# Kernel optimization log

Measured on AMD Instinct MI355X. Metric: run time of the kernel, lower is better.

The kernel has to match this reference:

```python
import jax, jax.numpy as jnp
import numpy as np

B, N, D, H, R = 4, 2048, 256, 8, 64
DH = D // H          # head dim = 32
K_SPARSE = 32        # top-k neighbors kept per query row
BN_EPS = 1e-5


def setup_inputs() -> dict:
    key = jax.random.key(0)
    ks = jax.random.split(key, 16)
    s_in = 1.0 / np.sqrt(D)
    s_r = 1.0 / np.sqrt(R)
    def lr(k1, k2):
        return (jax.random.normal(k1, (D, R), jnp.float32) * s_in,
                jax.random.normal(k2, (R, D), jnp.float32) * s_r)
    U_np, V_np = lr(ks[0], ks[1])
    U_q, V_q = lr(ks[2], ks[3])
    U_k, V_k = lr(ks[4], ks[5])
    U_v, V_v = lr(ks[6], ks[7])
    U_o, V_o = lr(ks[8], ks[9])
    U_op, V_op = lr(ks[10], ks[11])
    return {
        'x': jax.random.normal(ks[12], (B, N, D), jnp.float32),
        'U_np': U_np, 'V_np': V_np, 'b_np': jnp.zeros((D,), jnp.float32),
        'U_q': U_q, 'V_q': V_q,
        'U_k': U_k, 'V_k': V_k,
        'U_v': U_v, 'V_v': V_v,
        'U_o': U_o, 'V_o': V_o, 'b_o': jnp.zeros((D,), jnp.float32),
        'U_op': U_op, 'V_op': V_op, 'b_op': jnp.zeros((D,), jnp.float32),
        'gamma': jnp.ones((D,), jnp.float32),
        'beta': jnp.zeros((D,), jnp.float32),
    }


def _low_rank(x, U, V, b=None):
    y = (x @ U) @ V  # [..., D] -> [..., R] -> [..., D]
    return y + b if b is not None else y


def _heads(t):  # [B,N,D] -> [B,H,N,DH]
    return t.reshape(B, N, H, DH).transpose(0, 2, 1, 3)


def reference(x, U_np, V_np, b_np, U_q, V_q, U_k, V_k, U_v, V_v,
              U_o, V_o, b_o, U_op, V_op, b_op, gamma, beta):
    # node_proj: low-rank projection
    h = _low_rank(x, U_np, V_np, b_np)                      # [B,N,D]
    # low-rank sparse attention (q=k=v=h)
    q = _heads(_low_rank(h, U_q, V_q))                      # [B,H,N,DH]
    k = _heads(_low_rank(h, U_k, V_k))
    v = _heads(_low_rank(h, U_v, V_v))
    scores = jnp.einsum('bhnd,bhmd->bhnm', q, k) / jnp.sqrt(jnp.float32(DH))
    # topk sparsity: keep the K_SPARSE largest scores per query row
    thr = jax.lax.top_k(scores, K_SPARSE)[0][..., -1:]      # [B,H,N,1]
    neg_inf = jnp.finfo(scores.dtype).min
    scores = jnp.where(scores >= thr, scores, neg_inf)
    attn = jax.nn.softmax(scores, axis=-1)                  # [B,H,N,N]
    o = jnp.einsum('bhnm,bhmd->bhnd', attn, v)              # [B,H,N,DH]
    o = o.transpose(0, 2, 1, 3).reshape(B, N, D)
    o = _low_rank(o, U_o, V_o, b_o)                         # attention out proj
    # out_proj
    out = _low_rank(o, U_op, V_op, b_op)                    # [B,N,D]
    # BatchNorm1d over channel dim (stats over B and N, training-mode batch stats)
    mu = out.mean(axis=(0, 1))
    var = out.var(axis=(0, 1))
    out = (out - mu) * jax.lax.rsqrt(var + BN_EPS) * gamma + beta
    return out
```

## Files before the change

kernel.cpp:

```cpp
#include <hip/hip_runtime.h>
#include <hip/hip_bf16.h>

#define BB 4
#define NN 2048
#define DD 256
#define HH 8
#define RR 64
#define DHH 32
#define KSP 32
#define ROWS (BB*NN)
#define NEG_INF (-3.0e38f)

typedef __attribute__((ext_vector_type(8))) short bf16x8;
typedef __attribute__((ext_vector_type(4))) float f32x4;
#define MFMA16(A,B,C) __builtin_amdgcn_mfma_f32_16x16x32_bf16((A),(B),(C),0,0,0)

__global__ __launch_bounds__(64) void k_node_proj(
    const float* __restrict__ x, const float* __restrict__ U,
    const float* __restrict__ V, const float* __restrict__ bias,
    float* __restrict__ h)
{
    const int row = blockIdx.x, lane = threadIdx.x;
    __shared__ float xs[DD];
    __shared__ float ts[RR];
    const float* xr = x + (size_t)row * DD;
    { float4 t4 = ((const float4*)xr)[lane];
      xs[lane*4]=t4.x; xs[lane*4+1]=t4.y; xs[lane*4+2]=t4.z; xs[lane*4+3]=t4.w; }
    __syncthreads();
    float t = 0.f;
    for (int d = 0; d < DD; ++d) t = fmaf(xs[d], U[d*RR + lane], t);
    ts[lane] = t;
    __syncthreads();
    float a[4];
    #pragma unroll
    for (int j = 0; j < 4; ++j) a[j] = bias[lane + 64*j];
    for (int r = 0; r < RR; ++r) {
        float tv = ts[r];
        const float* Vr = V + r*DD + lane;
        #pragma unroll
        for (int j = 0; j < 4; ++j) a[j] = fmaf(tv, Vr[64*j], a[j]);
    }
    float* hr = h + (size_t)row * DD;
    #pragma unroll
    for (int j = 0; j < 4; ++j) hr[lane + 64*j] = a[j];
}

__global__ __launch_bounds__(64) void k_qkv(
    const float* __restrict__ h,
    const float* __restrict__ Uq, const float* __restrict__ Vq,
    const float* __restrict__ Uk, const float* __restrict__ Vk,
    const float* __restrict__ Uv, const float* __restrict__ Vv,
    float* __restrict__ q, float* __restrict__ k, float* __restrict__ v)
{
    const int row = blockIdx.x, lane = threadIdx.x;
    __shared__ float hs[DD];
    __shared__ float tq[RR], tk[RR], tvv[RR];
    const float* hr = h + (size_t)row * DD;
    { float4 t4 = ((const float4*)hr)[lane];
      hs[lane*4]=t4.x; hs[lane*4+1]=t4.y; hs[lane*4+2]=t4.z; hs[lane*4+3]=t4.w; }
    __syncthreads();
    float aq=0.f, ak=0.f, av=0.f;
    for (int d = 0; d < DD; ++d) {
        float hv = hs[d];
        aq = fmaf(hv, Uq[d*RR + lane], aq);
        ak = fmaf(hv, Uk[d*RR + lane], ak);
        av = fmaf(hv, Uv[d*RR + lane], av);
    }
    tq[lane]=aq; tk[lane]=ak; tvv[lane]=av;
    __syncthreads();
    float oq[4], ok[4], ov[4];
    #pragma unroll
    for (int j = 0; j < 4; ++j) { oq[j]=0.f; ok[j]=0.f; ov[j]=0.f; }
    for (int r = 0; r < RR; ++r) {
        float sq=tq[r], sk=tk[r], sv=tvv[r];
        const int base = r*DD + lane;
        #pragma unroll
        for (int j = 0; j < 4; ++j) {
            oq[j] = fmaf(sq, Vq[base + 64*j], oq[j]);
            ok[j] = fmaf(sk, Vk[base + 64*j], ok[j]);
            ov[j] = fmaf(sv, Vv[base + 64*j], ov[j]);
        }
    }
    float* qr = q + (size_t)row * DD;
    float* kr = k + (size_t)row * DD;
    float* vr = v + (size_t)row * DD;
    #pragma unroll
    for (int j = 0; j < 4; ++j) {
        qr[lane + 64*j] = oq[j];
        kr[lane + 64*j] = ok[j];
        vr[lane + 64*j] = ov[j];
    }
}

#define INSERT32(tp, sm) do { \
    _Pragma("unroll") for (int _i = 0; _i < 31; ++_i) \
        (tp)[_i] = __builtin_amdgcn_fmed3f((sm), (tp)[_i], (tp)[_i+1]); \
    (tp)[31] = fmaxf((tp)[31], (sm)); \
} while (0)

__device__ __forceinline__ unsigned short f2bf(float x) {
    __hip_bfloat16 h = __float2bfloat16(x);
    return *reinterpret_cast<unsigned short*>(&h);
}
__device__ __forceinline__ float bf2f(unsigned short u) {
    __hip_bfloat16 h; *reinterpret_cast<unsigned short*>(&h) = u;
    return __bfloat162float(h);
}
__device__ __forceinline__ void split3(float x, unsigned short& b1,
                                       unsigned short& b2, unsigned short& b3) {
    b1 = f2bf(x);        float f1 = bf2f(b1);
    float r = x - f1;    b2 = f2bf(r);
    float f2 = bf2f(b2); float r2 = r - f2;
    b3 = f2bf(r2);
}

__global__ __launch_bounds__(256)
__attribute__((amdgpu_waves_per_eu(3, 3)))
void k_attn(
    const float* __restrict__ qx, const float* __restrict__ kx,
    const float* __restrict__ vx, float* __restrict__ o)
{
    __shared__ float arena[4][2688];
    __shared__ float swl[256];
    const int tid  = threadIdx.x;
    const int lane = tid & 63;
    const int wv   = tid >> 6;
    const int blk  = blockIdx.x;
    const int tile = blk & 31;
    const int head = (blk >> 5) & 7;
    const int b    = blk >> 8;
    const float scale = 0.17677669529663687f;

    float* aw  = arena[wv];
    unsigned int* kbu = (unsigned int*)aw;
    float* scW = aw + 960;
    float* vbW = aw + 2112;

    const float* Kb = kx + (size_t)b*NN*DD + head*DHH;
    const float* Vb = vx + (size_t)b*NN*DD + head*DHH;
    const int j0 = wv*512;

    bf16x8 aq[4][3];
    {
        const int qr = lane & 15, ko = (lane >> 4) * 8;
        const float* qbase = qx + ((size_t)(b*NN + tile*64))*DD + head*DHH + ko;
        #pragma unroll
        for (int t = 0; t < 4; ++t) {
            const float* qp = qbase + (size_t)(t*16 + qr)*DD;
            float4 x0 = ((const float4*)qp)[0];
            float4 x1 = ((const float4*)qp)[1];
            float xv[8] = {x0.x,x0.y,x0.z,x0.w,x1.x,x1.y,x1.z,x1.w};
            #pragma unroll
            for (int i = 0; i < 8; ++i) {
                unsigned short u1,u2,u3;
                split3(xv[i]*scale, u1, u2, u3);
                aq[t][0][i] = (short)u1;
                aq[t][1][i] = (short)u2;
                aq[t][2][i] = (short)u3;
            }
        }
    }

    const int skey = lane >> 2, sgrp = lane & 3;
    const float* kSrc = Kb + (size_t)skey*DD + sgrp*8;
    const float* vSrc = Vb + (size_t)skey*DD + sgrp*8;

    auto convwrite_k = [&](float4 f0, float4 f1) {
        float xv[8] = {f0.x,f0.y,f0.z,f0.w,f1.x,f1.y,f1.z,f1.w};
        unsigned int w1[4], w2[4], w3[4];
        #pragma unroll
        for (int i = 0; i < 4; ++i) {
            unsigned short a0,b0,c0,a1,b1,c1;
            split3(xv[2*i],   a0, b0, c0);
            split3(xv[2*i+1], a1, b1, c1);
            w1[i] = (unsigned int)a0 | ((unsigned int)a1 << 16);
            w2[i] = (unsigned int)b0 | ((unsigned int)b1 << 16);
            w3[i] = (unsigned int)c0 | ((unsigned int)c1 << 16);
        }
        *(uint4*)(kbu + ( 0 + skey)*20 + sgrp*4) = make_uint4(w1[0],w1[1],w1[2],w1[3]);
        *(uint4*)(kbu + (16 + skey)*20 + sgrp*4) = make_uint4(w2[0],w2[1],w2[2],w2[3]);
        *(uint4*)(kbu + (32 + skey)*20 + sgrp*4) = make_uint4(w3[0],w3[1],w3[2],w3[3]);
    };

    auto scores_chunk = [&]() {
        const unsigned short* kb16 = (const unsigned short*)kbu;
        const int key = lane & 15, ko = (lane >> 4) * 8;
        bf16x8 bk0 = *(const bf16x8*)(kb16 + ( 0 + key)*40 + ko);
        bf16x8 bk1 = *(const bf16x8*)(kb16 + (16 + key)*40 + ko);
        bf16x8 bk2 = *(const bf16x8*)(kb16 + (32 + key)*40 + ko);
        const int qr0 = (lane >> 4) * 4;
        #pragma unroll
        for (int t = 0; t < 4; ++t) {
            f32x4 c4 = {0.f, 0.f, 0.f, 0.f};
            c4 = MFMA16(aq[t][0], bk0, c4);
            c4 = MFMA16(aq[t][0], bk1, c4);
            c4 = MFMA16(aq[t][1], bk0, c4);
            c4 = MFMA16(aq[t][0], bk2, c4);
            c4 = MFMA16(aq[t][2], bk0, c4);
            c4 = MFMA16(aq[t][1], bk1, c4);
            #pragma unroll
            for (int r = 0; r < 4; ++r)
                scW[(t*16 + qr0 + r)*18 + key] = c4[r];
        }
    };

    float t32[32];
    #pragma unroll
    for (int i = 0; i < 32; ++i) t32[i] = NEG_INF;

    {
        float4 k0, k1;
        { const float* p = kSrc + (size_t)j0*DD;
          k0 = ((const float4*)p)[0]; k1 = ((const float4*)p)[1]; }
        convwrite_k(k0, k1);
        for (int c = 0; c < 32; ++c) {
            if (c + 1 < 32) {
                const float* p = kSrc + (size_t)(j0 + (c+1)*16)*DD;
                k0 = ((const float4*)p)[0]; k1 = ((const float4*)p)[1];
            }
            scores_chunk();
            const float2* sp = (const float2*)(scW + lane*18);
            #pragma unroll
            for (int i = 0; i < 8; ++i) {
                float2 s2 = sp[i];
                INSERT32(t32, s2.x);
                INSERT32(t32, s2.y);
            }
            if (c + 1 < 32) convwrite_k(k0, k1);
        }
    }
    #pragma unroll
    for (int i = 0; i < 32; ++i) aw[i*64 + lane] = t32[i];
    __syncthreads();

    int i0=31, i1=31, i2=31, i3=31;
    float m = NEG_INF, thr = NEG_INF;
    for (int p = 0; p < 32; ++p) {
        float v0 = arena[0][i0*64 + lane];
        float v1 = arena[1][i1*64 + lane];
        float v2 = arena[2][i2*64 + lane];
        float v3 = arena[3][i3*64 + lane];
        float vm = fmaxf(fmaxf(v0,v1), fmaxf(v2,v3));
        if (p == 0) m = vm;
        thr = vm;
        if      (vm == v0) --i0;
        else if (vm == v1) --i1;
        else if (vm == v2) --i2;
        else               --i3;
    }
    __syncthreads();

    float acc[32];
    #pragma unroll
    for (int d = 0; d < 32; ++d) acc[d] = 0.f;
    float sw = 0.f;

    {
        float4 k0, k1, v0, v1;
        { const float* p = kSrc + (size_t)j0*DD;
          k0 = ((const float4*)p)[0]; k1 = ((const float4*)p)[1]; }
        { const float* p = vSrc + (size_t)j0*DD;
          v0 = ((const float4*)p)[0]; v1 = ((const float4*)p)[1]; }
        convwrite_k(k0, k1);
        { float* wp = vbW + skey*36 + sgrp*8;
          *(float4*)wp = v0; *(float4*)(wp + 4) = v1; }
        for (int c = 0; c < 32; ++c) {
            if (c + 1 < 32) {
                const float* p = kSrc + (size_t)(j0 + (c+1)*16)*DD;
                k0 = ((const float4*)p)[0]; k1 = ((const float4*)p)[1];
                const float* pv = vSrc + (size_t)(j0 + (c+1)*16)*DD;
                v0 = ((const float4*)pv)[0]; v1 = ((const float4*)pv)[1];
            }
            scores_chunk();
            const float2* sp = (const float2*)(scW + lane*18);
            #pragma unroll
            for (int i = 0; i < 8; ++i) {
                float2 s2 = sp[i];
                #pragma unroll
                for (int hs = 0; hs < 2; ++hs) {
                    float s = hs ? s2.y : s2.x;
                    int kk = 2*i + hs;
                    bool sel = (s >= thr);
                    float w = sel ? __expf(s - m) : 0.f;
                    sw += w;
                    if (__any(sel)) {
                        const float4* vv = (const float4*)(vbW + kk*36);
                        #pragma unroll
                        for (int r = 0; r < 8; ++r) {
                            float4 vvv = vv[r];
                            acc[4*r]   = fmaf(w, vvv.x, acc[4*r]);
                            acc[4*r+1] = fmaf(w, vvv.y, acc[4*r+1]);
                            acc[4*r+2] = fmaf(w, vvv.z, acc[4*r+2]);
                            acc[4*r+3] = fmaf(w, vvv.w, acc[4*r+3]);
                        }
                    }
                }
            }
            if (c + 1 < 32) {
                convwrite_k(k0, k1);
                float* wp = vbW + skey*36 + sgrp*8;
                *(float4*)wp = v0; *(float4*)(wp + 4) = v1;
            }
        }
    }

    #pragma unroll
    for (int d = 0; d < 32; ++d) aw[d*64 + lane] = acc[d];
    swl[wv*64 + lane] = sw;
    __syncthreads();

    float swsum = swl[lane] + swl[64+lane] + swl[128+lane] + swl[192+lane];
    float inv = 1.0f / swsum;
    float* orow = o + ((size_t)(b*NN + tile*64 + lane))*DD + head*DHH;
    #pragma unroll
    for (int dd = 0; dd < 8; ++dd) {
        int d = 8*wv + dd;
        float sv = arena[0][d*64+lane] + arena[1][d*64+lane]
                 + arena[2][d*64+lane] + arena[3][d*64+lane];
        orow[d] = sv * inv;
    }
}

__global__ __launch_bounds__(64) void k_out_proj(
    const float* __restrict__ o,
    const float* __restrict__ Uo,  const float* __restrict__ Vo,  const float* __restrict__ bo,
    const float* __restrict__ Uop, const float* __restrict__ Vop, const float* __restrict__ bop,
    float* __restrict__ outp)
{
    const int row = blockIdx.x, lane = threadIdx.x;
    __shared__ float buf[DD];
    __shared__ float ts[RR];
    const float* orow = o + (size_t)row * DD;
    { float4 t4 = ((const float4*)orow)[lane];
      buf[lane*4]=t4.x; buf[lane*4+1]=t4.y; buf[lane*4+2]=t4.z; buf[lane*4+3]=t4.w; }
    __syncthreads();
    float t = 0.f;
    for (int d = 0; d < DD; ++d) t = fmaf(buf[d], Uo[d*RR + lane], t);
    ts[lane] = t;
    __syncthreads();
    float a[4];
    #pragma unroll
    for (int j = 0; j < 4; ++j) a[j] = bo[lane + 64*j];
    for (int r = 0; r < RR; ++r) {
        float tv = ts[r];
        #pragma unroll
        for (int j = 0; j < 4; ++j) a[j] = fmaf(tv, Vo[r*DD + lane + 64*j], a[j]);
    }
    __syncthreads();
    #pragma unroll
    for (int j = 0; j < 4; ++j) buf[lane + 64*j] = a[j];
    __syncthreads();
    float t2 = 0.f;
    for (int d = 0; d < DD; ++d) t2 = fmaf(buf[d], Uop[d*RR + lane], t2);
    __syncthreads();
    ts[lane] = t2;
    __syncthreads();
    float c[4];
    #pragma unroll
    for (int j = 0; j < 4; ++j) c[j] = bop[lane + 64*j];
    for (int r = 0; r < RR; ++r) {
        float tv = ts[r];
        #pragma unroll
        for (int j = 0; j < 4; ++j) c[j] = fmaf(tv, Vop[r*DD + lane + 64*j], c[j]);
    }
    float* orow_out = outp + (size_t)row * DD;
    #pragma unroll
    for (int j = 0; j < 4; ++j) orow_out[lane + 64*j] = c[j];
}

__global__ __launch_bounds__(256) void k_bnstats(
    const float* __restrict__ outp, float* __restrict__ stats,
    const float* __restrict__ gamma, const float* __restrict__ beta)
{
    const int c = blockIdx.x, t = threadIdx.x;
    float s = 0.f, s2 = 0.f;
    for (int r = t; r < ROWS; r += 256) {
        float v = outp[(size_t)r*DD + c];
        s += v; s2 += v*v;
    }
    __shared__ float rs[256], rs2[256];
    rs[t] = s; rs2[t] = s2;
    __syncthreads();
    for (int step = 128; step; step >>= 1) {
        if (t < step) { rs[t] += rs[t+step]; rs2[t] += rs2[t+step]; }
        __syncthreads();
    }
    if (t == 0) {
        float mean = rs[0] * (1.0f/ROWS);
        float var  = rs2[0] * (1.0f/ROWS) - mean*mean;
        float inv  = rsqrtf(var + 1e-5f);
        float g = gamma[c], be = beta[c];
        stats[c]      = g * inv;
        stats[DD + c] = be - mean * g * inv;
    }
}

__global__ __launch_bounds__(256) void k_bnapply(
    const float* __restrict__ outp, const float* __restrict__ stats,
    float* __restrict__ out)
{
    const size_t idx = (size_t)blockIdx.x * 256 + threadIdx.x;
    const int c = (int)(idx & (DD-1));
    out[idx] = outp[idx] * stats[c] + stats[DD + c];
}

extern "C" void kernel_launch(void* const* d_in, const int* in_sizes, int n_in,
                              void* d_out, int out_size, void* d_ws, size_t ws_size,
                              hipStream_t stream)
{
    (void)in_sizes; (void)n_in; (void)out_size; (void)ws_size;
    const float* x    = (const float*)d_in[0];
    const float* U_np = (const float*)d_in[1];
    const float* V_np = (const float*)d_in[2];
    const float* b_np = (const float*)d_in[3];
    const float* U_q  = (const float*)d_in[4];
    const float* V_q  = (const float*)d_in[5];
    const float* U_k  = (const float*)d_in[6];
    const float* V_k  = (const float*)d_in[7];
    const float* U_v  = (const float*)d_in[8];
    const float* V_v  = (const float*)d_in[9];
    const float* U_o  = (const float*)d_in[10];
    const float* V_o  = (const float*)d_in[11];
    const float* b_o  = (const float*)d_in[12];
    const float* U_op = (const float*)d_in[13];
    const float* V_op = (const float*)d_in[14];
    const float* b_op = (const float*)d_in[15];
    const float* gamma= (const float*)d_in[16];
    const float* beta = (const float*)d_in[17];

    float* ws  = (float*)d_ws;
    float* out = (float*)d_out;
    const size_t BUF = (size_t)ROWS * DD;

    float* h    = out;
    float* q    = ws;
    float* k    = ws + BUF;
    float* v    = ws + 2*BUF;
    float* o    = out;
    float* outp = q;
    float* stats= k;

    k_node_proj<<<ROWS, 64, 0, stream>>>(x, U_np, V_np, b_np, h);
    k_qkv<<<ROWS, 64, 0, stream>>>(h, U_q, V_q, U_k, V_k, U_v, V_v, q, k, v);
    k_attn<<<BB*HH*32, 256, 0, stream>>>(q, k, v, o);
    k_out_proj<<<ROWS, 64, 0, stream>>>(o, U_o, V_o, b_o, U_op, V_op, b_op, outp);
    k_bnstats<<<DD, 256, 0, stream>>>(outp, stats, gamma, beta);
    k_bnapply<<<ROWS, 256, 0, stream>>>(outp, stats, out);
}
```

Measured before the change: 531.8 us.

## Replace per-score top-32 insertion with bitonic batch merge and split BN stats

Per-lane top-32 maintenance in the attention kernel now sorts each batch of 16 scores with a sorting network and merges it into the running sorted list. This replaces 16 full 32-element median-insertions per chunk. The per-wave LDS arena is shrunk by aliasing the K staging and score buffers, and occupancy is raised from 3 to 4 waves per EU. BatchNorm statistics move from a strided per-channel reduction to a coalesced two-stage partial-sum reduction. The trade-off is higher register pressure from the sorting network under a tighter wave budget, plus a reuse of the K staging region for scores.

Measured after the change: 512.0 us. 1.04x faster.

```diff
diff --git a/kernel.cpp b/kernel.cpp
--- a/kernel.cpp
+++ b/kernel.cpp
@@ -92,12 +92,6 @@
     }
 }
 
-#define INSERT32(tp, sm) do { \
-    _Pragma("unroll") for (int _i = 0; _i < 31; ++_i) \
-        (tp)[_i] = __builtin_amdgcn_fmed3f((sm), (tp)[_i], (tp)[_i+1]); \
-    (tp)[31] = fmaxf((tp)[31], (sm)); \
-} while (0)
-
 __device__ __forceinline__ unsigned short f2bf(float x) {
     __hip_bfloat16 h = __float2bfloat16(x);
     return *reinterpret_cast<unsigned short*>(&h);
@@ -114,13 +108,15 @@
     b3 = f2bf(r2);
 }
 
+#define CEX(a_, b_) { float _l = fminf(a_, b_); (b_) = fmaxf(a_, b_); (a_) = _l; }
+
 __global__ __launch_bounds__(256)
-__attribute__((amdgpu_waves_per_eu(3, 3)))
+__attribute__((amdgpu_waves_per_eu(4, 4)))
 void k_attn(
     const float* __restrict__ qx, const float* __restrict__ kx,
     const float* __restrict__ vx, float* __restrict__ o)
 {
-    __shared__ float arena[4][2688];
+    __shared__ float arena[4][2048];
     __shared__ float swl[256];
     const int tid  = threadIdx.x;
     const int lane = tid & 63;
@@ -133,8 +129,8 @@
 
     float* aw  = arena[wv];
     unsigned int* kbu = (unsigned int*)aw;
-    float* scW = aw + 960;
-    float* vbW = aw + 2112;
+    float* scW = aw;
+    float* vbW = aw + 1152;
 
     const float* Kb = kx + (size_t)b*NN*DD + head*DHH;
     const float* Vb = vx + (size_t)b*NN*DD + head*DHH;
@@ -204,6 +200,56 @@
         }
     };
 
+    auto merge_batch = [&](float* t, float* sb) {
+        #pragma unroll
+        for (int i = 0; i < 8; ++i) CEX(sb[2*i], sb[2*i+1]);
+        #pragma unroll
+        for (int g = 0; g < 4; ++g) { CEX(sb[4*g], sb[4*g+2]); CEX(sb[4*g+1], sb[4*g+3]); }
+        #pragma unroll
+        for (int g = 0; g < 4; ++g) CEX(sb[4*g+1], sb[4*g+2]);
+        #pragma unroll
+        for (int g = 0; g < 2; ++g) {
+            CEX(sb[8*g],   sb[8*g+4]); CEX(sb[8*g+1], sb[8*g+5]);
+            CEX(sb[8*g+2], sb[8*g+6]); CEX(sb[8*g+3], sb[8*g+7]);
+        }
+        #pragma unroll
+        for (int g = 0; g < 2; ++g) { CEX(sb[8*g+2], sb[8*g+4]); CEX(sb[8*g+3], sb[8*g+5]); }
+        #pragma unroll
+        for (int g = 0; g < 2; ++g) {
+            CEX(sb[8*g+1], sb[8*g+2]); CEX(sb[8*g+3], sb[8*g+4]); CEX(sb[8*g+5], sb[8*g+6]);
+        }
+        #pragma unroll
+        for (int i = 0; i < 8; ++i) CEX(sb[i], sb[i+8]);
+        #pragma unroll
+        for (int i = 0; i < 4; ++i) CEX(sb[i+4], sb[i+8]);
+        #pragma unroll
+        for (int g = 0; g < 3; ++g) { CEX(sb[4*g+2], sb[4*g+4]); CEX(sb[4*g+3], sb[4*g+5]); }
+        #pragma unroll
+        for (int i = 0; i < 7; ++i) CEX(sb[2*i+1], sb[2*i+2]);
+        float u[16];
+        #pragma unroll
+        for (int i = 0; i < 16; ++i) u[i] = fmaxf(t[i], sb[15-i]);
+        #pragma unroll
+        for (int st = 8; st >= 1; st >>= 1)
+            #pragma unroll
+            for (int i = 0; i < 16; ++i)
+                if ((i & st) == 0) CEX(u[i], u[i+st]);
+        #pragma unroll
+        for (int i = 0; i < 8; ++i) {
+            float hi1 = t[31-i], hi2 = t[16+i];
+            float u1 = u[i],     u2 = u[15-i];
+            t[i]    = fminf(u1, hi1);
+            t[31-i] = fmaxf(u1, hi1);
+            t[15-i] = fminf(u2, hi2);
+            t[16+i] = fmaxf(u2, hi2);
+        }
+        #pragma unroll
+        for (int st = 8; st >= 1; st >>= 1)
+            #pragma unroll
+            for (int i = 0; i < 32; ++i)
+                if ((i & st) == 0) CEX(t[i], t[i+st]);
+    };
+
     float t32[32];
     #pragma unroll
     for (int i = 0; i < 32; ++i) t32[i] = NEG_INF;
@@ -219,12 +265,12 @@
                 k0 = ((const float4*)p)[0]; k1 = ((const float4*)p)[1];
             }
             scores_chunk();
-            const float2* sp = (const float2*)(scW + lane*18);
-            #pragma unroll
-            for (int i = 0; i < 8; ++i) {
-                float2 s2 = sp[i];
-                INSERT32(t32, s2.x);
-                INSERT32(t32, s2.y);
+            {
+                const float2* sp = (const float2*)(scW + lane*18);
+                float sb[16];
+                #pragma unroll
+                for (int i = 0; i < 8; ++i) { float2 v2 = sp[i]; sb[2*i] = v2.x; sb[2*i+1] = v2.y; }
+                merge_batch(t32, sb);
             }
             if (c + 1 < 32) convwrite_k(k0, k1);
         }
@@ -368,31 +414,37 @@
     for (int j = 0; j < 4; ++j) orow_out[lane + 64*j] = c[j];
 }
 
-__global__ __launch_bounds__(256) void k_bnstats(
-    const float* __restrict__ outp, float* __restrict__ stats,
+__global__ __launch_bounds__(256) void k_bnpart(
+    const float* __restrict__ outp, float* __restrict__ part)
+{
+    const int blk = blockIdx.x, t = threadIdx.x;
+    const float* p = outp + (size_t)blk*64*DD + t;
+    float s = 0.f, s2 = 0.f;
+    #pragma unroll 4
+    for (int r = 0; r < 64; ++r) {
+        float v = p[(size_t)r*DD];
+        s += v; s2 += v*v;
+    }
+    part[blk*512 + t]       = s;
+    part[blk*512 + 256 + t] = s2;
+}
+
+__global__ __launch_bounds__(256) void k_bnfin(
+    const float* __restrict__ part, float* __restrict__ stats,
     const float* __restrict__ gamma, const float* __restrict__ beta)
 {
-    const int c = blockIdx.x, t = threadIdx.x;
+    const int c = threadIdx.x;
     float s = 0.f, s2 = 0.f;
-    for (int r = t; r < ROWS; r += 256) {
-        float v = outp[(size_t)r*DD + c];
-        s += v; s2 += v*v;
-    }
-    __shared__ float rs[256], rs2[256];
-    rs[t] = s; rs2[t] = s2;
-    __syncthreads();
-    for (int step = 128; step; step >>= 1) {
-        if (t < step) { rs[t] += rs[t+step]; rs2[t] += rs2[t+step]; }
-        __syncthreads();
-    }
-    if (t == 0) {
-        float mean = rs[0] * (1.0f/ROWS);
-        float var  = rs2[0] * (1.0f/ROWS) - mean*mean;
-        float inv  = rsqrtf(var + 1e-5f);
-        float g = gamma[c], be = beta[c];
-        stats[c]      = g * inv;
-        stats[DD + c] = be - mean * g * inv;
-    }
+    for (int j = 0; j < 128; ++j) {
+        s  += part[j*512 + c];
+        s2 += part[j*512 + 256 + c];
+    }
+    float mean = s * (1.0f/ROWS);
+    float var  = s2 * (1.0f/ROWS) - mean*mean;
+    float inv  = rsqrtf(var + 1e-5f);
+    float g = gamma[c], be = beta[c];
+    stats[c]      = g * inv;
+    stats[DD + c] = be - mean * g * inv;
 }
 
 __global__ __launch_bounds__(256) void k_bnapply(
@@ -439,11 +491,13 @@
     float* o    = out;
     float* outp = q;
     float* stats= k;
+    float* part = v;
 
     k_node_proj<<<ROWS, 64, 0, stream>>>(x, U_np, V_np, b_np, h);
     k_qkv<<<ROWS, 64, 0, stream>>>(h, U_q, V_q, U_k, V_k, U_v, V_v, q, k, v);
     k_attn<<<BB*HH*32, 256, 0, stream>>>(q, k, v, o);
     k_out_proj<<<ROWS, 64, 0, stream>>>(o, U_o, V_o, b_o, U_op, V_op, b_op, outp);
-    k_bnstats<<<DD, 256, 0, stream>>>(outp, stats, gamma, beta);
+    k_bnpart<<<128, 256, 0, stream>>>(outp, part);
+    k_bnfin<<<1, 256, 0, stream>>>(part, stats, gamma, beta);
     k_bnapply<<<ROWS, 256, 0, stream>>>(outp, stats, out);
 }
```
